# Kernel optimization log

Hardware: AMD Instinct MI355X
Metric: run time of the kernel (lower is better)

Reference implementation:

```python
import jax, jax.numpy as jnp
from jax import lax
import numpy as np

EPS = 1e-5


def conv2d(x, w, b, stride, pad):
    y = lax.conv_general_dilated(x, w, (stride, stride), [(pad, pad), (pad, pad)],
                                 dimension_numbers=('NCHW', 'OIHW', 'NCHW'))
    return y + b[None, :, None, None]


def conv_transpose2d(x, w, b, stride, pad, opad):
    # w in torch ConvTranspose2d layout: (Cin, Cout, kH, kW)
    k = w.shape[2]
    w_f = jnp.flip(w, (2, 3)).transpose(1, 0, 2, 3)  # -> OIHW
    lo = k - 1 - pad
    y = lax.conv_general_dilated(x, w_f, (1, 1), [(lo, lo + opad), (lo, lo + opad)],
                                 lhs_dilation=(stride, stride),
                                 dimension_numbers=('NCHW', 'OIHW', 'NCHW'))
    return y + b[None, :, None, None]


def batchnorm(x, g, b):
    # training-mode BN: batch statistics over (N, H, W)
    mean = jnp.mean(x, axis=(0, 2, 3), keepdims=True)
    var = jnp.var(x, axis=(0, 2, 3), keepdims=True)
    return (x - mean) * lax.rsqrt(var + EPS) * g[None, :, None, None] + b[None, :, None, None]


def quantize(z, codebook):
    # z: (B, C, H, W), codebook: (K, C)
    B, C, H, W = z.shape
    zf = z.transpose(0, 2, 3, 1).reshape(-1, C)  # (B*H*W, C)
    # squared Euclidean distances (argmin-equivalent to torch.cdist p=2)
    d2 = (jnp.sum(zf * zf, axis=1, keepdims=True)
          - 2.0 * zf @ codebook.T
          + jnp.sum(codebook * codebook, axis=1)[None, :])
    idx = jnp.argmin(d2, axis=-1)                # (B*H*W,)
    quant = codebook[idx]                        # gather
    loss_embed = jnp.mean((lax.stop_gradient(zf) - quant) ** 2)
    loss_commit = jnp.mean((zf - lax.stop_gradient(quant)) ** 2)
    quant_out = zf + lax.stop_gradient(quant - zf)  # straight-through
    quant_out = quant_out.reshape(B, H, W, C).transpose(0, 3, 1, 2)
    return quant_out, loss_embed, loss_commit, idx.reshape(B, H * W)


def setup_inputs() -> dict:
    key = jax.random.key(0)
    ks = jax.random.split(key, 20)
    f32 = jnp.float32

    def w(k, shape):
        fan_in = int(np.prod(shape[1:]))
        return jax.random.normal(k, shape, f32) / np.sqrt(fan_in)

    B, IMG = 64, 128
    C0, C1, C2, LAT, K = 3, 128, 256, 64, 512
    return {
        'x': jax.random.normal(ks[0], (B, C0, IMG, IMG), f32),
        'enc1_w': w(ks[1], (C1, C0, 3, 3)), 'enc1_b': jnp.zeros((C1,), f32),
        'bn1_g': jnp.ones((C1,), f32), 'bn1_b': jnp.zeros((C1,), f32),
        'enc2_w': w(ks[2], (C2, C1, 3, 3)), 'enc2_b': jnp.zeros((C2,), f32),
        'pre_w': w(ks[3], (LAT, C2, 1, 1)), 'pre_b': jnp.zeros((LAT,), f32),
        'codebook': jax.random.normal(ks[4], (K, LAT), f32),
        'post_w': w(ks[5], (C2, LAT, 1, 1)), 'post_b': jnp.zeros((C2,), f32),
        'dec1_w': w(ks[6], (C2, C1, 3, 3)), 'dec1_b': jnp.zeros((C1,), f32),
        'dbn1_g': jnp.ones((C1,), f32), 'dbn1_b': jnp.zeros((C1,), f32),
        'dec2_w': w(ks[7], (C1, C0, 3, 3)), 'dec2_b': jnp.zeros((C0,), f32),
    }


def reference(x, enc1_w, enc1_b, bn1_g, bn1_b, enc2_w, enc2_b, pre_w, pre_b,
              codebook, post_w, post_b, dec1_w, dec1_b, dbn1_g, dbn1_b,
              dec2_w, dec2_b):
    # encoder
    h = jax.nn.relu(batchnorm(conv2d(x, enc1_w, enc1_b, 2, 1), bn1_g, bn1_b))
    h = conv2d(h, enc2_w, enc2_b, 2, 1)          # (B, 256, 32, 32), no BN/act on last enc conv
    z = conv2d(h, pre_w, pre_b, 1, 0)            # (B, 64, 32, 32)
    # VQ codebook lookup
    q, loss_embed, loss_commit, idx = quantize(z, codebook)
    # decoder
    d = conv2d(q, post_w, post_b, 1, 0)          # (B, 256, 32, 32)
    d = jax.nn.relu(batchnorm(conv_transpose2d(d, dec1_w, dec1_b, 2, 1, 1), dbn1_g, dbn1_b))
    recon = jnp.tanh(conv_transpose2d(d, dec2_w, dec2_b, 2, 1, 1))  # (B, 3, 128, 128)
    return recon, loss_embed, loss_commit, idx
```

## Files before the change

### kernel.cpp

```cpp
#include <hip/hip_runtime.h>

#define EPS 1e-5f

typedef __attribute__((ext_vector_type(8))) short short8;
typedef __attribute__((ext_vector_type(4))) float f32x4;
typedef _Float16 half8v __attribute__((ext_vector_type(8)));

__device__ inline ushort f2bf(float f) {
    uint u = __float_as_uint(f);
    u += 0x7FFFu + ((u >> 16) & 1u);
    return (ushort)(u >> 16);
}
__device__ inline float bf2f(ushort h) { return __uint_as_float(((uint)h) << 16); }
__device__ inline ushort hbits(_Float16 h) { return __builtin_bit_cast(ushort, h); }

#define WS_LOSS     512
#define WS_BN1SC    1024
#define WS_BN1SH    1152
#define WS_BN2SC    1280
#define WS_BN2SH    1408
#define WS_CC       1536
#define WS_IDX      2048
#define WS_WT3      67584
#define WS_WT1      83968
#define WS_WT2      378880
#define WS_F        673792
#define WS_BN2S8    804864
#define WS_BN1S8    806912
#define WS_WTE1     808960
#define WS_CBS      819200
#define WS_A        1048576
#define WS_B        34603008
#define WS_Z        WS_A

#define OUT_LOSS_E  3145728
#define OUT_LOSS_C  3145729
#define OUT_IDX     3145730

__global__ __launch_bounds__(256) void k_wt(const float* __restrict__ dec1_w,
                                            const float* __restrict__ enc2_w,
                                            const float* __restrict__ pre_w,
                                            const float* __restrict__ enc1_w,
                                            const float* __restrict__ codebook,
                                            float* __restrict__ ws) {
    int g = blockIdx.x * 256 + threadIdx.x;
    if (g < 294912) {
        int ci = g & 255, co = (g >> 8) & 127, tap = g >> 15;
        float v = dec1_w[ci * 1152 + co * 9 + tap];
        ushort hi = f2bf(v);
        ushort lo = f2bf(v - bf2f(hi));
        ushort* u16 = (ushort*)(ws + WS_WT1);
        u16[g] = hi;
        u16[294912 + g] = lo;
    } else if (g < 2 * 294912) {
        int h = g - 294912;
        int ci = h & 127, rest = h >> 7;
        int co = rest & 255, tap = rest >> 8;
        float v = enc2_w[co * 1152 + ci * 9 + tap];
        _Float16 hi = (_Float16)v;
        _Float16 lo = (_Float16)((v - (float)hi) * 2048.0f);
        ushort* u16 = (ushort*)(ws + WS_WT2);
        u16[h] = hbits(hi);
        u16[294912 + h] = hbits(lo);
    } else if (g < 2 * 294912 + 16384) {
        int h = g - 2 * 294912;
        int co = h & 63, ci = h >> 6;
        ws[WS_WT3 + h] = pre_w[co * 256 + ci];
    } else if (g < 2 * 294912 + 16384 + 4096) {
        int h = g - (2 * 294912 + 16384);
        int k = h & 31, co = h >> 5;
        float v = (k < 27) ? enc1_w[co * 27 + k] : 0.f;
        _Float16 hi = (_Float16)v;
        _Float16 lo = (_Float16)((v - (float)hi) * 2048.0f);
        ushort* u16 = (ushort*)(ws + WS_WTE1);
        u16[h] = hbits(hi);
        u16[4096 + h] = hbits(lo);
    } else if (g < 2 * 294912 + 16384 + 4096 + 32768) {
        int h = g - (2 * 294912 + 16384 + 4096);
        float v = codebook[h];
        _Float16 hi = (_Float16)v;
        _Float16 lo = (_Float16)((v - (float)hi) * 2048.0f);
        ushort* u16 = (ushort*)(ws + WS_CBS);
        u16[h] = hbits(hi);
        u16[32768 + h] = hbits(lo);
    }
}

__global__ __launch_bounds__(256) void k_F(const float* __restrict__ codebook,
                                           const float* __restrict__ post_w,
                                           const float* __restrict__ post_b,
                                           float* __restrict__ ws) {
    __shared__ __align__(16) float cbr[64];
    int k = blockIdx.x, co = threadIdx.x;
    if (co < 64) cbr[co] = codebook[k * 64 + co];
    __syncthreads();
    float acc = post_b[co];
#pragma unroll
    for (int i = 0; i < 64; i += 4) {
        float4 w4 = *(const float4*)&post_w[co * 64 + i];
        acc = fmaf(cbr[i], w4.x, acc);
        acc = fmaf(cbr[i + 1], w4.y, acc);
        acc = fmaf(cbr[i + 2], w4.z, acc);
        acc = fmaf(cbr[i + 3], w4.w, acc);
    }
    ws[WS_F + k * 256 + co] = acc;
    if (co == 0) {
        float s = 0.f;
        for (int i = 0; i < 64; i++) s += cbr[i] * cbr[i];
        ws[WS_CC + k] = s;
    }
}

__global__ __launch_bounds__(256, 2) void k_enc1(const float* __restrict__ x,
                                                 const float* __restrict__ bias,
                                                 float* __restrict__ ws) {
    __shared__ __align__(16) float raw_s[1950];
    __shared__ __align__(16) ushort As_h[5120], As_l[5120];
    int b = blockIdx.x;
    int n = b >> 5, oy0 = (b & 31) * 2;
    int tid = threadIdx.x, lane = tid & 63, wid = tid >> 6;
    int wy = wid >> 1, wx = wid & 1;
    int l15 = lane & 15, quad = lane >> 4;
    int co0 = wx * 64;
    const ushort* we1h = (const ushort*)(ws + WS_WTE1);
    const ushort* we1l = we1h + 4096;

    half8v Bh[4], Bl[4];
#pragma unroll
    for (int nt = 0; nt < 4; nt++) {
        int src = (co0 + nt * 16 + l15) * 32 + quad * 8;
        Bh[nt] = *(const half8v*)&we1h[src];
        Bl[nt] = *(const half8v*)&we1l[src];
    }

    for (int i = tid; i < 1950; i += 256) {
        int c = i % 130, rest = i / 130;
        int rr = rest % 5, ci = rest / 5;
        int iy = 2 * oy0 - 1 + rr, ix = c - 1;
        float v = 0.f;
        if ((unsigned)iy < 128u && (unsigned)ix < 128u)
            v = x[(n * 3 + ci) * 16384 + iy * 128 + ix];
        raw_s[i] = v;
    }
    __syncthreads();

    for (int i = tid; i < 4096; i += 256) {
        int m = i >> 5, k = i & 31;
        float v = 0.f;
        if (k < 27) {
            int ci = k / 9, t9 = k - ci * 9;
            int ky = t9 / 3, kx = t9 - ky * 3;
            int r = m >> 6, xx = m & 63;
            v = raw_s[(ci * 5 + 2 * r + ky) * 130 + 2 * xx + kx];
        }
        _Float16 hi = (_Float16)v;
        _Float16 lo = (_Float16)((v - (float)hi) * 2048.f);
        As_h[m * 40 + k] = hbits(hi);
        As_l[m * 40 + k] = hbits(lo);
    }
    __syncthreads();

    f32x4 acc1[4][4], acc2[4][4];
#pragma unroll
    for (int nt = 0; nt < 4; nt++) {
        float bv = bias[co0 + nt * 16 + l15];
#pragma unroll
        for (int mt = 0; mt < 4; mt++) {
            acc1[mt][nt] = (f32x4){bv, bv, bv, bv};
            acc2[mt][nt] = (f32x4){0.f, 0.f, 0.f, 0.f};
        }
    }

    half8v Ah[4], Al[4];
#pragma unroll
    for (int mt = 0; mt < 4; mt++) {
        int aoff = (wy * 64 + mt * 16 + l15) * 40 + quad * 8;
        Ah[mt] = *(const half8v*)&As_h[aoff];
        Al[mt] = *(const half8v*)&As_l[aoff];
    }
#pragma unroll
    for (int nt = 0; nt < 4; nt++)
#pragma unroll
        for (int mt = 0; mt < 4; mt++) {
            acc2[mt][nt] = __builtin_amdgcn_mfma_f32_16x16x32_f16(Ah[mt], Bl[nt], acc2[mt][nt], 0, 0, 0);
            acc2[mt][nt] = __builtin_amdgcn_mfma_f32_16x16x32_f16(Al[mt], Bh[nt], acc2[mt][nt], 0, 0, 0);
            acc1[mt][nt] = __builtin_amdgcn_mfma_f32_16x16x32_f16(Ah[mt], Bh[nt], acc1[mt][nt], 0, 0, 0);
        }

    float* h1 = ws + WS_A;
    const float ls = 1.f / 2048.f;
    int oy = oy0 + wy;
#pragma unroll
    for (int mt = 0; mt < 4; mt++) {
        int x0 = mt * 16 + quad * 4;
#pragma unroll
        for (int nt = 0; nt < 4; nt++) {
            int co = co0 + nt * 16 + l15;
            *(float4*)&h1[((n * 128 + co) * 64 + oy) * 64 + x0] =
                make_float4(fmaf(acc2[mt][nt][0], ls, acc1[mt][nt][0]),
                            fmaf(acc2[mt][nt][1], ls, acc1[mt][nt][1]),
                            fmaf(acc2[mt][nt][2], ls, acc1[mt][nt][2]),
                            fmaf(acc2[mt][nt][3], ls, acc1[mt][nt][3]));
        }
    }
    int shadow = (b & 7) * 256;
#pragma unroll
    for (int nt = 0; nt < 4; nt++) {
        float s1 = 0.f, s2 = 0.f;
#pragma unroll
        for (int mt = 0; mt < 4; mt++)
#pragma unroll
            for (int r = 0; r < 4; r++) {
                float v = fmaf(acc2[mt][nt][r], ls, acc1[mt][nt][r]);
                s1 += v; s2 += v * v;
            }
        s1 += __shfl_xor(s1, 16); s1 += __shfl_xor(s1, 32);
        s2 += __shfl_xor(s2, 16); s2 += __shfl_xor(s2, 32);
        if (quad == 0) {
            int co = co0 + nt * 16 + l15;
            atomicAdd(&ws[WS_BN1S8 + shadow + co], s1);
            atomicAdd(&ws[WS_BN1S8 + shadow + 128 + co], s2);
        }
    }
}

__global__ __launch_bounds__(128) void k_bnfin8(const float* __restrict__ sums8,
                                                const float* __restrict__ g,
                                                const float* __restrict__ b,
                                                float* __restrict__ scale,
                                                float* __restrict__ shift) {
    int c = threadIdx.x;
    float s1 = 0.f, s2 = 0.f;
    for (int k = 0; k < 8; k++) {
        s1 += sums8[k * 256 + c];
        s2 += sums8[k * 256 + 128 + c];
    }
    float mean = s1 * (1.f / 262144.f);
    float var = s2 * (1.f / 262144.f) - mean * mean;
    float sc = g[c] * rsqrtf(var + EPS);
    scale[c] = sc;
    shift[c] = b[c] - mean * sc;
}

__global__ __launch_bounds__(256, 2) void k_enc2(const float* __restrict__ bias,
                                                 float* __restrict__ ws) {
    __shared__ __align__(16) uint As_h[6500], As_l[6500];
    __shared__ float scs[128], shs[128];
    int b = blockIdx.x;
    int n = b >> 4, y0 = (b & 15) * 2;
    int tid = threadIdx.x, lane = tid & 63, wid = tid >> 6;
    int l15 = lane & 15, quad = lane >> 4;
    int co0 = wid * 64;
    const float* h1 = ws + WS_A;
    const ushort* w2h = (const ushort*)(ws + WS_WT2);
    const ushort* w2l = w2h + 294912;

    if (tid < 128) { scs[tid] = ws[WS_BN1SC + tid]; shs[tid] = ws[WS_BN1SH + tid]; }

    int Abase[4];
#pragma unroll
    for (int mt = 0; mt < 4; mt++) {
        int m = mt * 16 + l15;
        Abase[mt] = (2 * (m >> 5)) * 2600 + (2 * (m & 31)) * 40 + quad * 8;
    }

    f32x4 acc1[4][4], acc2[4][4];
#pragma unroll
    for (int nt = 0; nt < 4; nt++) {
        float bv = bias[co0 + nt * 16 + l15];
#pragma unroll
        for (int mt = 0; mt < 4; mt++) {
            acc1[mt][nt] = (f32x4){bv, bv, bv, bv};
            acc2[mt][nt] = (f32x4){0.f, 0.f, 0.f, 0.f};
        }
    }

    for (int c0 = 0; c0 < 128; c0 += 32) {
        __syncthreads();
        if (tid < 80) {
            int p = tid & 15, row = tid >> 4;
            As_h[row * 1300 + p] = 0;
            As_l[row * 1300 + p] = 0;
        }
        for (int i = tid; i < 1280; i += 256) {
            int p = i & 15, g = i >> 4;
            int row = g >> 4, colg = g & 15;
            int in_y = 2 * y0 - 1 + row;
            int ci0 = c0 + 2 * p;
            float av[4] = {0.f, 0.f, 0.f, 0.f}, bv[4] = {0.f, 0.f, 0.f, 0.f};
            if ((unsigned)in_y < 64u) {
                const float* bp = h1 + (n * 128 + ci0) * 4096 + in_y * 64 + colg * 4;
                float4 va = *(const float4*)bp;
                float4 vb = *(const float4*)(bp + 4096);
                float sa = scs[ci0], ta = shs[ci0];
                float sb = scs[ci0 + 1], tb = shs[ci0 + 1];
                av[0] = fmaxf(fmaf(va.x, sa, ta), 0.f); av[1] = fmaxf(fmaf(va.y, sa, ta), 0.f);
                av[2] = fmaxf(fmaf(va.z, sa, ta), 0.f); av[3] = fmaxf(fmaf(va.w, sa, ta), 0.f);
                bv[0] = fmaxf(fmaf(vb.x, sb, tb), 0.f); bv[1] = fmaxf(fmaf(vb.y, sb, tb), 0.f);
                bv[2] = fmaxf(fmaf(vb.z, sb, tb), 0.f); bv[3] = fmaxf(fmaf(vb.w, sb, tb), 0.f);
            }
            int wbase = row * 1300 + (colg * 4 + 1) * 20 + p;
#pragma unroll
            for (int j = 0; j < 4; j++) {
                _Float16 ah = (_Float16)av[j], bh = (_Float16)bv[j];
                _Float16 al = (_Float16)((av[j] - (float)ah) * 2048.f);
                _Float16 bl = (_Float16)((bv[j] - (float)bh) * 2048.f);
                As_h[wbase + j * 20] = (uint)hbits(ah) | ((uint)hbits(bh) << 16);
                As_l[wbase + j * 20] = (uint)hbits(al) | ((uint)hbits(bl) << 16);
            }
        }
        __syncthreads();
        const ushort* ah16 = (const ushort*)As_h;
        const ushort* al16 = (const ushort*)As_l;
#pragma unroll
        for (int tap = 0; tap < 9; tap++) {
            int ky = tap / 3, kx = tap - ky * 3;
            int toff = ky * 2600 + kx * 40;
            half8v Bh[4], Bl[4];
#pragma unroll
            for (int nt = 0; nt < 4; nt++) {
                int src = (tap * 256 + co0 + nt * 16 + l15) * 128 + c0 + quad * 8;
                Bh[nt] = *(const half8v*)&w2h[src];
                Bl[nt] = *(const half8v*)&w2l[src];
            }
            half8v Ah[4], Al[4];
#pragma unroll
            for (int mt = 0; mt < 4; mt++) {
                Ah[mt] = *(const half8v*)&ah16[Abase[mt] + toff];
                Al[mt] = *(const half8v*)&al16[Abase[mt] + toff];
            }
#pragma unroll
            for (int nt = 0; nt < 4; nt++)
#pragma unroll
                for (int mt = 0; mt < 4; mt++) {
                    acc2[mt][nt] = __builtin_amdgcn_mfma_f32_16x16x32_f16(Ah[mt], Bl[nt], acc2[mt][nt], 0, 0, 0);
                    acc2[mt][nt] = __builtin_amdgcn_mfma_f32_16x16x32_f16(Al[mt], Bh[nt], acc2[mt][nt], 0, 0, 0);
                    acc1[mt][nt] = __builtin_amdgcn_mfma_f32_16x16x32_f16(Ah[mt], Bh[nt], acc1[mt][nt], 0, 0, 0);
                }
        }
    }

    float* h2 = ws + WS_B;
    const float ls = 1.f / 2048.f;
#pragma unroll
    for (int mt = 0; mt < 4; mt++) {
        int mloc = mt * 16 + quad * 4;
        int y = y0 + (mloc >> 5), x = mloc & 31;
#pragma unroll
        for (int nt = 0; nt < 4; nt++) {
            int co = co0 + nt * 16 + l15;
            *(float4*)&h2[(n * 256 + co) * 1024 + y * 32 + x] =
                make_float4(fmaf(acc2[mt][nt][0], ls, acc1[mt][nt][0]),
                            fmaf(acc2[mt][nt][1], ls, acc1[mt][nt][1]),
                            fmaf(acc2[mt][nt][2], ls, acc1[mt][nt][2]),
                            fmaf(acc2[mt][nt][3], ls, acc1[mt][nt][3]));
        }
    }
}

__global__ __launch_bounds__(256) void k_pre(const float* __restrict__ bias,
                                             float* __restrict__ ws) {
    __shared__ __align__(16) float a_s[8 * 128];
    __shared__ __align__(16) float b_s[8 * 64];
    int p0 = blockIdx.x * 128;
    int n = p0 >> 10, sp0 = p0 & 1023;
    int tid = threadIdx.x;
    int px4 = tid & 31, cg = tid >> 5;
    int co8 = cg * 8;
    const float* h2 = ws + WS_B;
    const float* wt3 = ws + WS_WT3;

    float acc[4][8];
#pragma unroll
    for (int r = 0; r < 4; r++)
#pragma unroll
        for (int j = 0; j < 8; j++) acc[r][j] = bias[co8 + j];

    for (int c0 = 0; c0 < 256; c0 += 8) {
        __syncthreads();
#pragma unroll
        for (int it = 0; it < 4; it++) {
            int t = tid + it * 256;
            a_s[t] = h2[n * 262144 + (c0 + (t >> 7)) * 1024 + sp0 + (t & 127)];
        }
#pragma unroll
        for (int it = 0; it < 2; it++) {
            int t = tid + it * 256;
            b_s[t] = wt3[(c0 + (t >> 6)) * 64 + (t & 63)];
        }
        __syncthreads();
#pragma unroll
        for (int ci = 0; ci < 8; ci++) {
            float4 av = *(const float4*)&a_s[ci * 128 + px4 * 4];
            float4 w0 = *(const float4*)&b_s[ci * 64 + co8];
            float4 w1 = *(const float4*)&b_s[ci * 64 + co8 + 4];
            float wv[8] = {w0.x, w0.y, w0.z, w0.w, w1.x, w1.y, w1.z, w1.w};
            float a[4] = {av.x, av.y, av.z, av.w};
#pragma unroll
            for (int j = 0; j < 8; j++)
#pragma unroll
                for (int r = 0; r < 4; r++) acc[r][j] = fmaf(a[r], wv[j], acc[r][j]);
        }
    }
    float* z = ws + WS_Z;
#pragma unroll
    for (int r = 0; r < 4; r++) {
        int p = p0 + px4 * 4 + r;
        *(float4*)&z[p * 64 + co8] = make_float4(acc[r][0], acc[r][1], acc[r][2], acc[r][3]);
        *(float4*)&z[p * 64 + co8 + 4] = make_float4(acc[r][4], acc[r][5], acc[r][6], acc[r][7]);
    }
}

__global__ __launch_bounds__(256, 2) void k_vq(float* __restrict__ out,
                                               float* __restrict__ ws) {
    __shared__ __align__(16) ushort Ash[64 * 72], Asl[64 * 72];
    __shared__ float zz_s[64];
    __shared__ float red_s[256];
    __shared__ int red_i[256];
    int p0 = blockIdx.x * 64;
    int tid = threadIdx.x, lane = tid & 63, wid = tid >> 6;
    int l15 = lane & 15, quad = lane >> 4;
    const float* z = ws + WS_Z;
    const ushort* cbh = (const ushort*)(ws + WS_CBS);
    const ushort* cbl = cbh + 32768;

    for (int i = tid; i < 1024; i += 256) {
        int m = i >> 4, k4 = (i & 15) * 4;
        float4 v = *(const float4*)&z[(p0 + m) * 64 + k4];
        _Float16 h0 = (_Float16)v.x, h1 = (_Float16)v.y, h2 = (_Float16)v.z, h3 = (_Float16)v.w;
        _Float16 l0 = (_Float16)((v.x - (float)h0) * 2048.f);
        _Float16 l1 = (_Float16)((v.y - (float)h1) * 2048.f);
        _Float16 l2 = (_Float16)((v.z - (float)h2) * 2048.f);
        _Float16 l3 = (_Float16)((v.w - (float)h3) * 2048.f);
        int d = m * 72 + k4;
        *(uint*)&Ash[d]     = (uint)hbits(h0) | ((uint)hbits(h1) << 16);
        *(uint*)&Ash[d + 2] = (uint)hbits(h2) | ((uint)hbits(h3) << 16);
        *(uint*)&Asl[d]     = (uint)hbits(l0) | ((uint)hbits(l1) << 16);
        *(uint*)&Asl[d + 2] = (uint)hbits(l2) | ((uint)hbits(l3) << 16);
    }
    if (tid < 64) {
        const float* zp = &z[(p0 + tid) * 64];
        float s = 0.f;
#pragma unroll
        for (int k = 0; k < 64; k += 4) {
            float4 v = *(const float4*)&zp[k];
            s += v.x * v.x + v.y * v.y + v.z * v.z + v.w * v.w;
        }
        zz_s[tid] = s;
    }
    __syncthreads();

    float best_s[4][4];
    int best_i[4][4];
#pragma unroll
    for (int mt = 0; mt < 4; mt++)
#pragma unroll
        for (int r = 0; r < 4; r++) { best_s[mt][r] = 3.4e38f; best_i[mt][r] = 0; }

    const float ls = 1.f / 2048.f;
    for (int pass = 0; pass < 2; pass++) {
        f32x4 acc1[4][4], acc2[4][4];
#pragma unroll
        for (int mt = 0; mt < 4; mt++)
#pragma unroll
            for (int nt = 0; nt < 4; nt++) {
                acc1[mt][nt] = (f32x4){0.f, 0.f, 0.f, 0.f};
                acc2[mt][nt] = (f32x4){0.f, 0.f, 0.f, 0.f};
            }
#pragma unroll
        for (int kc = 0; kc < 2; kc++) {
            half8v Ah[4], Al[4];
#pragma unroll
            for (int mt = 0; mt < 4; mt++) {
                int aoff = (mt * 16 + l15) * 72 + kc * 32 + quad * 8;
                Ah[mt] = *(const half8v*)&Ash[aoff];
                Al[mt] = *(const half8v*)&Asl[aoff];
            }
#pragma unroll
            for (int nt = 0; nt < 4; nt++) {
                int code = wid * 128 + pass * 64 + nt * 16 + l15;
                int src = code * 64 + kc * 32 + quad * 8;
                half8v Bh = *(const half8v*)&cbh[src];
                half8v Bl = *(const half8v*)&cbl[src];
#pragma unroll
                for (int mt = 0; mt < 4; mt++) {
                    acc2[mt][nt] = __builtin_amdgcn_mfma_f32_16x16x32_f16(Ah[mt], Bl, acc2[mt][nt], 0, 0, 0);
                    acc2[mt][nt] = __builtin_amdgcn_mfma_f32_16x16x32_f16(Al[mt], Bh, acc2[mt][nt], 0, 0, 0);
                    acc1[mt][nt] = __builtin_amdgcn_mfma_f32_16x16x32_f16(Ah[mt], Bh, acc1[mt][nt], 0, 0, 0);
                }
            }
        }
#pragma unroll
        for (int nt = 0; nt < 4; nt++) {
            int code = wid * 128 + pass * 64 + nt * 16 + l15;
            float cc = ws[WS_CC + code];
#pragma unroll
            for (int mt = 0; mt < 4; mt++)
#pragma unroll
                for (int r = 0; r < 4; r++) {
                    float dot = fmaf(acc2[mt][nt][r], ls, acc1[mt][nt][r]);
                    float s = fmaf(-2.f, dot, cc);
                    if (s < best_s[mt][r] || (s == best_s[mt][r] && code < best_i[mt][r])) {
                        best_s[mt][r] = s; best_i[mt][r] = code;
                    }
                }
        }
    }

#pragma unroll
    for (int mt = 0; mt < 4; mt++)
#pragma unroll
        for (int r = 0; r < 4; r++) {
            float s = best_s[mt][r];
            int ix = best_i[mt][r];
#pragma unroll
            for (int off = 1; off < 16; off <<= 1) {
                float so = __shfl_xor(s, off);
                int io = __shfl_xor(ix, off);
                if (so < s || (so == s && io < ix)) { s = so; ix = io; }
            }
            if (l15 == 0) {
                int px = mt * 16 + quad * 4 + r;
                red_s[wid * 64 + px] = s;
                red_i[wid * 64 + px] = ix;
            }
        }
    __syncthreads();
    if (tid < 64) {
        float s = red_s[tid];
        int ix = red_i[tid];
#pragma unroll
        for (int w = 1; w < 4; w++) {
            float so = red_s[w * 64 + tid];
            int io = red_i[w * 64 + tid];
            if (so < s || (so == s && io < ix)) { s = so; ix = io; }
        }
        out[OUT_IDX + p0 + tid] = (float)ix;
        ((int*)(ws + WS_IDX))[p0 + tid] = ix;
        float e = fmaxf(zz_s[tid] + s, 0.f);
#pragma unroll
        for (int off = 32; off; off >>= 1) e += __shfl_down(e, off);
        if (tid == 0) atomicAdd(&ws[WS_LOSS], e);
    }
}

__global__ void k_loss(float* __restrict__ out, const float* __restrict__ ws) {
    if (threadIdx.x == 0) {
        float v = ws[WS_LOSS] * (1.f / (65536.f * 64.f));
        out[OUT_LOSS_E] = v;
        out[OUT_LOSS_C] = v;
    }
}

__global__ __launch_bounds__(256) void k_gather(float* __restrict__ ws) {
    int tid = threadIdx.x;
    const int* idx = (const int*)(ws + WS_IDX);
    const float* F = ws + WS_F;
    float* dpx = ws + WS_B;
    int base = blockIdx.x * 64;
    for (int i = 0; i < 64; i++) {
        int row = idx[base + i];
        dpx[(base + i) * 256 + tid] = F[row * 256 + tid];
    }
}

__global__ __launch_bounds__(256, 2) void k_dec1(const float* __restrict__ bias,
                                                 float* __restrict__ ws) {
    __shared__ __align__(16) short As_h[5280], As_l[5280];
    __shared__ __align__(16) short Bs_h[4096], Bs_l[4096];
    int bx = blockIdx.x;
    int tile = bx & 511, phase = bx >> 9;
    int py = phase >> 1, px = phase & 1;
    int n_img = tile >> 3, a0 = (tile & 7) * 4;
    int tid = threadIdx.x, lane = tid & 63, wid = tid >> 6;
    int wy = wid >> 1, wx = wid & 1;
    int l15 = lane & 15, quad = lane >> 4;

    int ntY = py + 1, ntX = px + 1, ntap = ntY * ntX;
    int tap_off[4], tap_w[4];
    {
        int ti = 0;
        for (int ty = 0; ty < ntY; ty++)
            for (int tx = 0; tx < ntX; tx++) {
                int dy = py ? 1 - ty : 0, ky = py ? 2 * ty : 1;
                int dx = px ? 1 - tx : 0, kx = px ? 2 * tx : 1;
                tap_off[ti] = (dy * 33 + dx) * 32;
                tap_w[ti] = ky * 3 + kx;
                ti++;
            }
    }

    int Aoff[4];
#pragma unroll
    for (int mt = 0; mt < 4; mt++) {
        int m_loc = wy * 64 + mt * 16 + l15;
        Aoff[mt] = ((m_loc >> 5) * 33 + (m_loc & 31)) * 32 + quad * 8;
    }
    int Boff[4];
#pragma unroll
    for (int nt = 0; nt < 4; nt++)
        Boff[nt] = (wx * 64 + nt * 16 + l15) * 32 + quad * 8;

    f32x4 acc[4][4];
#pragma unroll
    for (int nt = 0; nt < 4; nt++) {
        float bv = bias[wx * 64 + nt * 16 + l15];
#pragma unroll
        for (int mt = 0; mt < 4; mt++) acc[mt][nt] = (f32x4){bv, bv, bv, bv};
    }

    const float* dpx = ws + WS_B;
    const ushort* wbh = (const ushort*)(ws + WS_WT1);
    const ushort* wbl = wbh + 294912;

    for (int c0 = 0; c0 < 256; c0 += 32) {
        __syncthreads();
        for (int i = tid; i < 1320; i += 256) {
            int p5 = i >> 3, q = i & 7;
            int rr = p5 / 33, cc = p5 - rr * 33;
            int a_in = a0 + rr;
            float4 v = make_float4(0.f, 0.f, 0.f, 0.f);
            if (a_in < 32 && cc < 32)
                v = *(const float4*)&dpx[(n_img * 1024 + a_in * 32 + cc) * 256 + c0 + q * 4];
            ushort h0 = f2bf(v.x), h1 = f2bf(v.y), h2 = f2bf(v.z), h3v = f2bf(v.w);
            ushort l0 = f2bf(v.x - bf2f(h0)), l1 = f2bf(v.y - bf2f(h1));
            ushort l2 = f2bf(v.z - bf2f(h2)), l3 = f2bf(v.w - bf2f(h3v));
            int d = p5 * 32 + q * 4;
            *(uint*)&As_h[d]     = (uint)h0 | ((uint)h1 << 16);
            *(uint*)&As_h[d + 2] = (uint)h2 | ((uint)h3v << 16);
            *(uint*)&As_l[d]     = (uint)l0 | ((uint)l1 << 16);
            *(uint*)&As_l[d + 2] = (uint)l2 | ((uint)l3 << 16);
        }
        for (int t = 0; t < ntap; t++) {
            if (t) __syncthreads();
            int tw = tap_w[t];
            for (int i = tid; i < 512; i += 256) {
                int co = i >> 2, q = i & 3;
                int src = (tw * 128 + co) * 256 + c0 + q * 8;
                *(uint4*)&Bs_h[co * 32 + q * 8] = *(const uint4*)&wbh[src];
                *(uint4*)&Bs_l[co * 32 + q * 8] = *(const uint4*)&wbl[src];
            }
            __syncthreads();
            int ao = tap_off[t];
            short8 Ah[4], Al[4];
#pragma unroll
            for (int mt = 0; mt < 4; mt++) {
                Ah[mt] = *(const short8*)&As_h[Aoff[mt] + ao];
                Al[mt] = *(const short8*)&As_l[Aoff[mt] + ao];
            }
#pragma unroll
            for (int nt = 0; nt < 4; nt++) {
                short8 Bh = *(const short8*)&Bs_h[Boff[nt]];
                short8 Bl = *(const short8*)&Bs_l[Boff[nt]];
#pragma unroll
                for (int mt = 0; mt < 4; mt++) {
                    acc[mt][nt] = __builtin_amdgcn_mfma_f32_16x16x32_bf16(Ah[mt], Bh, acc[mt][nt], 0, 0, 0);
                    acc[mt][nt] = __builtin_amdgcn_mfma_f32_16x16x32_bf16(Ah[mt], Bl, acc[mt][nt], 0, 0, 0);
                    acc[mt][nt] = __builtin_amdgcn_mfma_f32_16x16x32_bf16(Al[mt], Bh, acc[mt][nt], 0, 0, 0);
                }
            }
        }
    }

    float* h3n = ws + WS_A;
#pragma unroll
    for (int mt = 0; mt < 4; mt++) {
#pragma unroll
        for (int r = 0; r < 4; r++) {
            int m_glob = tile * 128 + wy * 64 + mt * 16 + quad * 4 + r;
            int a = (m_glob >> 5) & 31, bb = m_glob & 31;
            int y = 2 * a + py, x = 2 * bb + px;
            float* rowp = &h3n[(((m_glob >> 10) * 64 + y) * 64 + x) * 128 + wx * 64];
#pragma unroll
            for (int nt = 0; nt < 4; nt++) rowp[nt * 16 + l15] = acc[mt][nt][r];
        }
    }
    int shadow = (bx & 7) * 256;
#pragma unroll
    for (int nt = 0; nt < 4; nt++) {
        float s1 = 0.f, s2 = 0.f;
#pragma unroll
        for (int mt = 0; mt < 4; mt++)
#pragma unroll
            for (int r = 0; r < 4; r++) {
                float v = acc[mt][nt][r];
                s1 += v; s2 += v * v;
            }
        s1 += __shfl_xor(s1, 16); s1 += __shfl_xor(s1, 32);
        s2 += __shfl_xor(s2, 16); s2 += __shfl_xor(s2, 32);
        if (quad == 0) {
            int co = wx * 64 + nt * 16 + l15;
            atomicAdd(&ws[WS_BN2S8 + shadow + co], s1);
            atomicAdd(&ws[WS_BN2S8 + shadow + 128 + co], s2);
        }
    }
}

__global__ __launch_bounds__(1024, 2) void k_dec2(const float* __restrict__ w,
                                                  const float* __restrict__ bias,
                                                  float* __restrict__ out,
                                                  float* __restrict__ ws) {
    __shared__ __align__(16) float in_s[8 * 5 * 66];
    __shared__ __align__(16) float w_s[8 * 9 * 3];
    __shared__ float scs[128], shs[128];
    int n = blockIdx.y;
    int atile = blockIdx.x;
    int a0 = atile * 4;
    int tid = threadIdx.x;
    int phase = tid >> 8;
    int py = phase >> 1, px = phase & 1;
    int tidl = tid & 255;
    int b = tidl & 63, r4 = tidl >> 6;
    int ntsh = py + px;
    int ntap = 1 << ntsh;
    const float* h3n = ws + WS_A;

    if (tid < 128) { scs[tid] = ws[WS_BN2SC + tid]; shs[tid] = ws[WS_BN2SH + tid]; }

    float acc[3] = {bias[0], bias[1], bias[2]};
    for (int c0 = 0; c0 < 128; c0 += 8) {
        __syncthreads();
        if (tid < 660) {
            int ciq = tid & 1, s = tid >> 1;
            int cL = s % 66, row = s / 66;
            int iy = a0 + row;
            float r0 = 0.f, r1 = 0.f, r2 = 0.f, r3 = 0.f;
            if (iy < 64 && cL < 64) {
                float4 v = *(const float4*)&h3n[((n * 64 + iy) * 64 + cL) * 128 + c0 + ciq * 4];
                int cb = c0 + ciq * 4;
                r0 = fmaxf(fmaf(v.x, scs[cb], shs[cb]), 0.f);
                r1 = fmaxf(fmaf(v.y, scs[cb + 1], shs[cb + 1]), 0.f);
                r2 = fmaxf(fmaf(v.z, scs[cb + 2], shs[cb + 2]), 0.f);
                r3 = fmaxf(fmaf(v.w, scs[cb + 3], shs[cb + 3]), 0.f);
            }
            int ci0 = ciq * 4;
            in_s[(ci0 + 0) * 330 + row * 66 + cL] = r0;
            in_s[(ci0 + 1) * 330 + row * 66 + cL] = r1;
            in_s[(ci0 + 2) * 330 + row * 66 + cL] = r2;
            in_s[(ci0 + 3) * 330 + row * 66 + cL] = r3;
        }
        if (tid < 8 * 9 * 3) {
            int co = tid % 3, q = tid / 3;
            int ci = q / 9, tap = q - ci * 9;
            w_s[q * 3 + co] = w[(c0 + ci) * 27 + co * 9 + tap];
        }
        __syncthreads();
#pragma unroll
        for (int ci = 0; ci < 8; ci++) {
#pragma unroll
            for (int tt = 0; tt < 4; tt++) {
                if (tt >= ntap) break;
                int ty = tt >> px, tx = tt & px;
                int ky = py ? 2 * ty : 1;
                int kx = px ? 2 * tx : 1;
                int dyv = py ? 1 - ty : 0;
                int dxv = px ? 1 - tx : 0;
                float v = in_s[ci * 330 + (r4 + dyv) * 66 + b + dxv];
                const float* wp = &w_s[(ci * 9 + ky * 3 + kx) * 3];
                acc[0] = fmaf(v, wp[0], acc[0]);
                acc[1] = fmaf(v, wp[1], acc[1]);
                acc[2] = fmaf(v, wp[2], acc[2]);
            }
        }
    }
    int y = 2 * (a0 + r4) + py, xcol = 2 * b + px;
#pragma unroll
    for (int co = 0; co < 3; co++)
        out[(n * 3 + co) * 16384 + y * 128 + xcol] = tanhf(acc[co]);
}

extern "C" void kernel_launch(void* const* d_in, const int* in_sizes, int n_in,
                              void* d_out, int out_size, void* d_ws, size_t ws_size,
                              hipStream_t stream) {
    const float* x       = (const float*)d_in[0];
    const float* enc1_w  = (const float*)d_in[1];
    const float* enc1_b  = (const float*)d_in[2];
    const float* bn1_g   = (const float*)d_in[3];
    const float* bn1_b   = (const float*)d_in[4];
    const float* enc2_w  = (const float*)d_in[5];
    const float* enc2_b  = (const float*)d_in[6];
    const float* pre_w   = (const float*)d_in[7];
    const float* pre_b   = (const float*)d_in[8];
    const float* codebook= (const float*)d_in[9];
    const float* post_w  = (const float*)d_in[10];
    const float* post_b  = (const float*)d_in[11];
    const float* dec1_w  = (const float*)d_in[12];
    const float* dec1_b  = (const float*)d_in[13];
    const float* dbn1_g  = (const float*)d_in[14];
    const float* dbn1_b  = (const float*)d_in[15];
    const float* dec2_w  = (const float*)d_in[16];
    const float* dec2_b  = (const float*)d_in[17];
    float* out = (float*)d_out;
    float* ws  = (float*)d_ws;

    hipMemsetAsync(ws, 0, 4096, stream);
    hipMemsetAsync(ws + WS_BN2S8, 0, 2 * 8 * 256 * 4, stream);

    k_wt<<<2512, 256, 0, stream>>>(dec1_w, enc2_w, pre_w, enc1_w, codebook, ws);
    k_F<<<512, 256, 0, stream>>>(codebook, post_w, post_b, ws);
    k_enc1<<<2048, 256, 0, stream>>>(x, enc1_b, ws);
    k_bnfin8<<<1, 128, 0, stream>>>(ws + WS_BN1S8, bn1_g, bn1_b,
                                    ws + WS_BN1SC, ws + WS_BN1SH);
    k_enc2<<<1024, 256, 0, stream>>>(enc2_b, ws);
    k_pre<<<512, 256, 0, stream>>>(pre_b, ws);
    k_vq<<<1024, 256, 0, stream>>>(out, ws);
    k_loss<<<1, 64, 0, stream>>>(out, ws);
    k_gather<<<1024, 256, 0, stream>>>(ws);
    k_dec1<<<2048, 256, 0, stream>>>(dec1_b, ws);
    k_bnfin8<<<1, 128, 0, stream>>>(ws + WS_BN2S8, dbn1_g, dbn1_b,
                                    ws + WS_BN2SC, ws + WS_BN2SH);
    k_dec2<<<dim3(16, 64), 1024, 0, stream>>>(dec2_w, dec2_b, out, ws);
}
```

Before: 695.9 us.

## Move pre-conv to split-fp16 MFMA, fuse gather into VQ, trim LDS use

The 1x1 pre-quant conv moves from scalar FMA to split hi/lo fp16 MFMA, with a new weight-split section added to the setup kernel. The codebook-feature gather now runs at the end of the VQ kernel, removing a separate launch. enc2 drops its LDS padding so three blocks can fit per CU. dec1 now loads weight fragments straight from global memory instead of staging them in LDS, which removes per-tap barriers but adds global loads. Each change trades some risk of bank conflicts or memory traffic for fewer barriers and better occupancy.

```diff
diff --git a/kernel.cpp b/kernel.cpp
--- a/kernel.cpp
+++ b/kernel.cpp
@@ -29,6 +29,7 @@
 #define WS_BN1S8    806912
 #define WS_WTE1     808960
 #define WS_CBS      819200
+#define WS_WT3S     851968
 #define WS_A        1048576
 #define WS_B        34603008
 #define WS_Z        WS_A
@@ -83,6 +84,14 @@
         ushort* u16 = (ushort*)(ws + WS_CBS);
         u16[h] = hbits(hi);
         u16[32768 + h] = hbits(lo);
+    } else if (g < 2 * 294912 + 16384 + 4096 + 32768 + 16384) {
+        int h = g - (2 * 294912 + 16384 + 4096 + 32768);
+        float v = pre_w[h];
+        _Float16 hi = (_Float16)v;
+        _Float16 lo = (_Float16)((v - (float)hi) * 2048.0f);
+        ushort* u16 = (ushort*)(ws + WS_WT3S);
+        u16[h] = hbits(hi);
+        u16[16384 + h] = hbits(lo);
     }
 }
 
@@ -242,9 +251,9 @@
     shift[c] = b[c] - mean * sc;
 }
 
-__global__ __launch_bounds__(256, 2) void k_enc2(const float* __restrict__ bias,
+__global__ __launch_bounds__(256, 3) void k_enc2(const float* __restrict__ bias,
                                                  float* __restrict__ ws) {
-    __shared__ __align__(16) uint As_h[6500], As_l[6500];
+    __shared__ __align__(16) uint As_h[5200], As_l[5200];
     __shared__ float scs[128], shs[128];
     int b = blockIdx.x;
     int n = b >> 4, y0 = (b & 15) * 2;
@@ -261,7 +270,7 @@
 #pragma unroll
     for (int mt = 0; mt < 4; mt++) {
         int m = mt * 16 + l15;
-        Abase[mt] = (2 * (m >> 5)) * 2600 + (2 * (m & 31)) * 40 + quad * 8;
+        Abase[mt] = (2 * (m >> 5)) * 2080 + (2 * (m & 31)) * 32 + quad * 8;
     }
 
     f32x4 acc1[4][4], acc2[4][4];
@@ -279,8 +288,8 @@
         __syncthreads();
         if (tid < 80) {
             int p = tid & 15, row = tid >> 4;
-            As_h[row * 1300 + p] = 0;
-            As_l[row * 1300 + p] = 0;
+            As_h[row * 1040 + p] = 0;
+            As_l[row * 1040 + p] = 0;
         }
         for (int i = tid; i < 1280; i += 256) {
             int p = i & 15, g = i >> 4;
@@ -299,14 +308,14 @@
                 bv[0] = fmaxf(fmaf(vb.x, sb, tb), 0.f); bv[1] = fmaxf(fmaf(vb.y, sb, tb), 0.f);
                 bv[2] = fmaxf(fmaf(vb.z, sb, tb), 0.f); bv[3] = fmaxf(fmaf(vb.w, sb, tb), 0.f);
             }
-            int wbase = row * 1300 + (colg * 4 + 1) * 20 + p;
+            int wbase = row * 1040 + (colg * 4 + 1) * 16 + p;
 #pragma unroll
             for (int j = 0; j < 4; j++) {
                 _Float16 ah = (_Float16)av[j], bh = (_Float16)bv[j];
                 _Float16 al = (_Float16)((av[j] - (float)ah) * 2048.f);
                 _Float16 bl = (_Float16)((bv[j] - (float)bh) * 2048.f);
-                As_h[wbase + j * 20] = (uint)hbits(ah) | ((uint)hbits(bh) << 16);
-                As_l[wbase + j * 20] = (uint)hbits(al) | ((uint)hbits(bl) << 16);
+                As_h[wbase + j * 16] = (uint)hbits(ah) | ((uint)hbits(bh) << 16);
+                As_l[wbase + j * 16] = (uint)hbits(al) | ((uint)hbits(bl) << 16);
             }
         }
         __syncthreads();
@@ -315,7 +324,7 @@
 #pragma unroll
         for (int tap = 0; tap < 9; tap++) {
             int ky = tap / 3, kx = tap - ky * 3;
-            int toff = ky * 2600 + kx * 40;
+            int toff = ky * 2080 + kx * 32;
             half8v Bh[4], Bl[4];
 #pragma unroll
             for (int nt = 0; nt < 4; nt++) {
@@ -358,57 +367,87 @@
     }
 }
 
-__global__ __launch_bounds__(256) void k_pre(const float* __restrict__ bias,
-                                             float* __restrict__ ws) {
-    __shared__ __align__(16) float a_s[8 * 128];
-    __shared__ __align__(16) float b_s[8 * 64];
+__global__ __launch_bounds__(256, 2) void k_pre(const float* __restrict__ bias,
+                                                float* __restrict__ ws) {
+    __shared__ __align__(16) uint As_h[2048], As_l[2048];
     int p0 = blockIdx.x * 128;
     int n = p0 >> 10, sp0 = p0 & 1023;
-    int tid = threadIdx.x;
-    int px4 = tid & 31, cg = tid >> 5;
-    int co8 = cg * 8;
+    int tid = threadIdx.x, lane = tid & 63, wid = tid >> 6;
+    int l15 = lane & 15, quad = lane >> 4;
     const float* h2 = ws + WS_B;
-    const float* wt3 = ws + WS_WT3;
-
-    float acc[4][8];
-#pragma unroll
-    for (int r = 0; r < 4; r++)
-#pragma unroll
-        for (int j = 0; j < 8; j++) acc[r][j] = bias[co8 + j];
-
-    for (int c0 = 0; c0 < 256; c0 += 8) {
+    const ushort* w3h = (const ushort*)(ws + WS_WT3S);
+    const ushort* w3l = w3h + 16384;
+
+    f32x4 acc1[2][4], acc2[2][4];
+#pragma unroll
+    for (int nt = 0; nt < 4; nt++) {
+        float bv = bias[nt * 16 + l15];
+#pragma unroll
+        for (int mt = 0; mt < 2; mt++) {
+            acc1[mt][nt] = (f32x4){bv, bv, bv, bv};
+            acc2[mt][nt] = (f32x4){0.f, 0.f, 0.f, 0.f};
+        }
+    }
+
+    for (int c0 = 0; c0 < 256; c0 += 32) {
         __syncthreads();
 #pragma unroll
-        for (int it = 0; it < 4; it++) {
-            int t = tid + it * 256;
-            a_s[t] = h2[n * 262144 + (c0 + (t >> 7)) * 1024 + sp0 + (t & 127)];
-        }
-#pragma unroll
         for (int it = 0; it < 2; it++) {
-            int t = tid + it * 256;
-            b_s[t] = wt3[(c0 + (t >> 6)) * 64 + (t & 63)];
+            int i = tid + it * 256;
+            int p = i & 15, g = i >> 4;
+            int ci0 = c0 + 2 * p;
+            const float* bp = h2 + (n * 256 + ci0) * 1024 + sp0 + g * 4;
+            float4 va = *(const float4*)bp;
+            float4 vb = *(const float4*)(bp + 1024);
+            float av[4] = {va.x, va.y, va.z, va.w};
+            float bv[4] = {vb.x, vb.y, vb.z, vb.w};
+#pragma unroll
+            for (int j = 0; j < 4; j++) {
+                _Float16 ah = (_Float16)av[j], bh = (_Float16)bv[j];
+                _Float16 al = (_Float16)((av[j] - (float)ah) * 2048.f);
+                _Float16 bl = (_Float16)((bv[j] - (float)bh) * 2048.f);
+                As_h[(g * 4 + j) * 16 + p] = (uint)hbits(ah) | ((uint)hbits(bh) << 16);
+                As_l[(g * 4 + j) * 16 + p] = (uint)hbits(al) | ((uint)hbits(bl) << 16);
+            }
         }
         __syncthreads();
-#pragma unroll
-        for (int ci = 0; ci < 8; ci++) {
-            float4 av = *(const float4*)&a_s[ci * 128 + px4 * 4];
-            float4 w0 = *(const float4*)&b_s[ci * 64 + co8];
-            float4 w1 = *(const float4*)&b_s[ci * 64 + co8 + 4];
-            float wv[8] = {w0.x, w0.y, w0.z, w0.w, w1.x, w1.y, w1.z, w1.w};
-            float a[4] = {av.x, av.y, av.z, av.w};
-#pragma unroll
-            for (int j = 0; j < 8; j++)
-#pragma unroll
-                for (int r = 0; r < 4; r++) acc[r][j] = fmaf(a[r], wv[j], acc[r][j]);
-        }
-    }
+        const ushort* ah16 = (const ushort*)As_h;
+        const ushort* al16 = (const ushort*)As_l;
+        half8v Bh[4], Bl[4];
+#pragma unroll
+        for (int nt = 0; nt < 4; nt++) {
+            int src = (nt * 16 + l15) * 256 + c0 + quad * 8;
+            Bh[nt] = *(const half8v*)&w3h[src];
+            Bl[nt] = *(const half8v*)&w3l[src];
+        }
+        half8v Ah[2], Al[2];
+#pragma unroll
+        for (int mt = 0; mt < 2; mt++) {
+            int aoff = (wid * 32 + mt * 16 + l15) * 32 + quad * 8;
+            Ah[mt] = *(const half8v*)&ah16[aoff];
+            Al[mt] = *(const half8v*)&al16[aoff];
+        }
+#pragma unroll
+        for (int nt = 0; nt < 4; nt++)
+#pragma unroll
+            for (int mt = 0; mt < 2; mt++) {
+                acc2[mt][nt] = __builtin_amdgcn_mfma_f32_16x16x32_f16(Ah[mt], Bl[nt], acc2[mt][nt], 0, 0, 0);
+                acc2[mt][nt] = __builtin_amdgcn_mfma_f32_16x16x32_f16(Al[mt], Bh[nt], acc2[mt][nt], 0, 0, 0);
+                acc1[mt][nt] = __builtin_amdgcn_mfma_f32_16x16x32_f16(Ah[mt], Bh[nt], acc1[mt][nt], 0, 0, 0);
+            }
+    }
+
     float* z = ws + WS_Z;
-#pragma unroll
-    for (int r = 0; r < 4; r++) {
-        int p = p0 + px4 * 4 + r;
-        *(float4*)&z[p * 64 + co8] = make_float4(acc[r][0], acc[r][1], acc[r][2], acc[r][3]);
-        *(float4*)&z[p * 64 + co8 + 4] = make_float4(acc[r][4], acc[r][5], acc[r][6], acc[r][7]);
-    }
+    const float ls = 1.f / 2048.f;
+#pragma unroll
+    for (int mt = 0; mt < 2; mt++)
+#pragma unroll
+        for (int r = 0; r < 4; r++) {
+            int px = p0 + wid * 32 + mt * 16 + quad * 4 + r;
+#pragma unroll
+            for (int nt = 0; nt < 4; nt++)
+                z[px * 64 + nt * 16 + l15] = fmaf(acc2[mt][nt][r], ls, acc1[mt][nt][r]);
+        }
 }
 
 __global__ __launch_bounds__(256, 2) void k_vq(float* __restrict__ out,
@@ -537,10 +576,22 @@
         }
         out[OUT_IDX + p0 + tid] = (float)ix;
         ((int*)(ws + WS_IDX))[p0 + tid] = ix;
+        red_i[tid] = ix;
         float e = fmaxf(zz_s[tid] + s, 0.f);
 #pragma unroll
         for (int off = 32; off; off >>= 1) e += __shfl_down(e, off);
         if (tid == 0) atomicAdd(&ws[WS_LOSS], e);
+    }
+    __syncthreads();
+    {
+        const float* F = ws + WS_F;
+        float* dpx = ws + WS_B;
+        int px = tid >> 2, cg = (tid & 3) * 64;
+        int row = red_i[px];
+        const float4* src4 = (const float4*)&F[row * 256 + cg];
+        float4* dst4 = (float4*)&dpx[(p0 + px) * 256 + cg];
+#pragma unroll
+        for (int i = 0; i < 16; i++) dst4[i] = src4[i];
     }
 }
 
@@ -552,22 +603,9 @@
     }
 }
 
-__global__ __launch_bounds__(256) void k_gather(float* __restrict__ ws) {
-    int tid = threadIdx.x;
-    const int* idx = (const int*)(ws + WS_IDX);
-    const float* F = ws + WS_F;
-    float* dpx = ws + WS_B;
-    int base = blockIdx.x * 64;
-    for (int i = 0; i < 64; i++) {
-        int row = idx[base + i];
-        dpx[(base + i) * 256 + tid] = F[row * 256 + tid];
-    }
-}
-
-__global__ __launch_bounds__(256, 2) void k_dec1(const float* __restrict__ bias,
+__global__ __launch_bounds__(256, 3) void k_dec1(const float* __restrict__ bias,
                                                  float* __restrict__ ws) {
     __shared__ __align__(16) short As_h[5280], As_l[5280];
-    __shared__ __align__(16) short Bs_h[4096], Bs_l[4096];
     int bx = blockIdx.x;
     int tile = bx & 511, phase = bx >> 9;
     int py = phase >> 1, px = phase & 1;
@@ -596,10 +634,6 @@
         int m_loc = wy * 64 + mt * 16 + l15;
         Aoff[mt] = ((m_loc >> 5) * 33 + (m_loc & 31)) * 32 + quad * 8;
     }
-    int Boff[4];
-#pragma unroll
-    for (int nt = 0; nt < 4; nt++)
-        Boff[nt] = (wx * 64 + nt * 16 + l15) * 32 + quad * 8;
 
     f32x4 acc[4][4];
 #pragma unroll
@@ -631,16 +665,16 @@
             *(uint*)&As_l[d]     = (uint)l0 | ((uint)l1 << 16);
             *(uint*)&As_l[d + 2] = (uint)l2 | ((uint)l3 << 16);
         }
+        __syncthreads();
         for (int t = 0; t < ntap; t++) {
-            if (t) __syncthreads();
             int tw = tap_w[t];
-            for (int i = tid; i < 512; i += 256) {
-                int co = i >> 2, q = i & 3;
-                int src = (tw * 128 + co) * 256 + c0 + q * 8;
-                *(uint4*)&Bs_h[co * 32 + q * 8] = *(const uint4*)&wbh[src];
-                *(uint4*)&Bs_l[co * 32 + q * 8] = *(const uint4*)&wbl[src];
-            }
-            __syncthreads();
+            short8 Bh[4], Bl[4];
+#pragma unroll
+            for (int nt = 0; nt < 4; nt++) {
+                int src = (tw * 128 + wx * 64 + nt * 16 + l15) * 256 + c0 + quad * 8;
+                Bh[nt] = *(const short8*)&wbh[src];
+                Bl[nt] = *(const short8*)&wbl[src];
+            }
             int ao = tap_off[t];
             short8 Ah[4], Al[4];
 #pragma unroll
@@ -649,16 +683,13 @@
                 Al[mt] = *(const short8*)&As_l[Aoff[mt] + ao];
             }
 #pragma unroll
-            for (int nt = 0; nt < 4; nt++) {
-                short8 Bh = *(const short8*)&Bs_h[Boff[nt]];
-                short8 Bl = *(const short8*)&Bs_l[Boff[nt]];
+            for (int nt = 0; nt < 4; nt++)
 #pragma unroll
                 for (int mt = 0; mt < 4; mt++) {
-                    acc[mt][nt] = __builtin_amdgcn_mfma_f32_16x16x32_bf16(Ah[mt], Bh, acc[mt][nt], 0, 0, 0);
-                    acc[mt][nt] = __builtin_amdgcn_mfma_f32_16x16x32_bf16(Ah[mt], Bl, acc[mt][nt], 0, 0, 0);
-                    acc[mt][nt] = __builtin_amdgcn_mfma_f32_16x16x32_bf16(Al[mt], Bh, acc[mt][nt], 0, 0, 0);
+                    acc[mt][nt] = __builtin_amdgcn_mfma_f32_16x16x32_bf16(Ah[mt], Bh[nt], acc[mt][nt], 0, 0, 0);
+                    acc[mt][nt] = __builtin_amdgcn_mfma_f32_16x16x32_bf16(Ah[mt], Bl[nt], acc[mt][nt], 0, 0, 0);
+                    acc[mt][nt] = __builtin_amdgcn_mfma_f32_16x16x32_bf16(Al[mt], Bh[nt], acc[mt][nt], 0, 0, 0);
                 }
-            }
         }
     }
 
@@ -796,7 +827,7 @@
     hipMemsetAsync(ws, 0, 4096, stream);
     hipMemsetAsync(ws + WS_BN2S8, 0, 2 * 8 * 256 * 4, stream);
 
-    k_wt<<<2512, 256, 0, stream>>>(dec1_w, enc2_w, pre_w, enc1_w, codebook, ws);
+    k_wt<<<2576, 256, 0, stream>>>(dec1_w, enc2_w, pre_w, enc1_w, codebook, ws);
     k_F<<<512, 256, 0, stream>>>(codebook, post_w, post_b, ws);
     k_enc1<<<2048, 256, 0, stream>>>(x, enc1_b, ws);
     k_bnfin8<<<1, 128, 0, stream>>>(ws + WS_BN1S8, bn1_g, bn1_b,
@@ -805,7 +836,6 @@
     k_pre<<<512, 256, 0, stream>>>(pre_b, ws);
     k_vq<<<1024, 256, 0, stream>>>(out, ws);
     k_loss<<<1, 64, 0, stream>>>(out, ws);
-    k_gather<<<1024, 256, 0, stream>>>(ws);
     k_dec1<<<2048, 256, 0, stream>>>(dec1_b, ws);
     k_bnfin8<<<1, 128, 0, stream>>>(ws + WS_BN2S8, dbn1_g, dbn1_b,
                                     ws + WS_BN2SC, ws + WS_BN2SH);
```

After: 1.011 ms. 45.3% more time.
